# Kernel optimization log

Hardware: AMD Instinct MI355X
Metric: run time of the kernel (lower is better)

Reference implementation:

```python
import jax, jax.numpy as jnp
import numpy as np

B, L, F, C, H, FF = 8, 64, 16, 128, 8, 512


def setup_inputs() -> dict:
    key = jax.random.key(0)
    ks = jax.random.split(key, 5)
    s = jnp.float32(0.02)
    return {
        "x": jax.random.normal(ks[0], (B, L, F, C), jnp.float32),
        "wq": jax.random.normal(ks[1], (C * H, C), jnp.float32) * s,
        "bq": jnp.zeros((C * H,), jnp.float32),
        "wk": jax.random.normal(ks[2], (C * H, C), jnp.float32) * s,
        "bk": jnp.zeros((C * H,), jnp.float32),
        "wv": jax.random.normal(ks[3], (C * H, C), jnp.float32) * s,
        "bv": jnp.zeros((C * H,), jnp.float32),
        "wo": jax.random.normal(ks[4], (C, C * H), jnp.float32) * s,
        "bo": jnp.zeros((C,), jnp.float32),
        "ln1_g": jnp.ones((C,), jnp.float32),
        "ln1_b": jnp.zeros((C,), jnp.float32),
        "w1": jax.random.normal(jax.random.fold_in(key, 10), (FF, C), jnp.float32) * s,
        "b1": jnp.zeros((FF,), jnp.float32),
        "w2": jax.random.normal(jax.random.fold_in(key, 11), (C, FF), jnp.float32) * s,
        "b2": jnp.zeros((C,), jnp.float32),
        "ln2_g": jnp.ones((C,), jnp.float32),
        "ln2_b": jnp.zeros((C,), jnp.float32),
    }


def _layer_norm(x, g, b, eps=1e-5):
    m = jnp.mean(x, axis=-1, keepdims=True)
    v = jnp.mean(jnp.square(x - m), axis=-1, keepdims=True)  # biased var, like torch LN
    return (x - m) * jax.lax.rsqrt(v + eps) * g + b


def reference(x, wq, bq, wk, bk, wv, bv, wo, bo, ln1_g, ln1_b, w1, b1, w2, b2, ln2_g, ln2_b):
    b_, l, f, c = x.shape
    h = wq.shape[0] // c  # num_heads

    def proj(w, bias):
        y = x @ w.T + bias                       # (B,L,F,C*H)
        y = y.reshape(b_, l, f, c, h)
        return jnp.transpose(y, (0, 4, 1, 2, 3))  # (B,H,L,F,C)

    q = proj(wq, bq)
    k = proj(wk, bk)
    v = proj(wv, bv)

    # scores over joint (L,F) query/key axes: (B,H,Lq,Fq,Lk,Fk)
    scores = jnp.einsum('bhlfc,bhmgc->bhlfmg', q, k) / jnp.sqrt(jnp.float32(c))
    # double softmax: first over key-L axis, then over key-F axis of the result
    a = jax.nn.softmax(scores, axis=4)
    a = jax.nn.softmax(a, axis=5)
    z = jnp.einsum('bhlfmg,bhmgc->bhlfc', a, v)   # (B,H,L,F,C)
    z = jnp.transpose(z, (0, 2, 3, 4, 1)).reshape(b_, l, f, c * h)
    attn_out = z @ wo.T + bo                      # (B,L,F,C)

    z1 = _layer_norm(attn_out + x, ln1_g, ln1_b)  # residual + LN1 (dropout=0, eval)
    ffy = jax.nn.relu(z1 @ w1.T + b1) @ w2.T + b2
    return _layer_norm(ffy + z1, ln2_g, ln2_b)
```

## Files before the change

### kernel.cpp

```cpp
#include <hip/hip_runtime.h>


typedef unsigned short u16;
typedef unsigned int u32;
typedef __attribute__((ext_vector_type(4))) float f32x4;
typedef __attribute__((ext_vector_type(8))) short s16x8;
typedef __attribute__((ext_vector_type(4))) unsigned short u16x4;

__device__ __forceinline__ u16 f2bf(float f) {
    union { float f; u32 u; } v; v.f = f;
    u32 u = v.u;
    u += 0x7fffu + ((u >> 16) & 1u);
    return (u16)(u >> 16);
}
__device__ __forceinline__ float bf2f(u16 h) {
    union { u32 u; float f; } v; v.u = ((u32)h) << 16;
    return v.f;
}
__device__ __forceinline__ u32 pack_trunc(float lo, float hi) {
    return __builtin_amdgcn_perm(__float_as_uint(hi), __float_as_uint(lo), 0x07060302u);
}
__device__ __forceinline__ s16x8 ldg8(const u16* p) { return *(const s16x8*)p; }

#define MFMA(a, b, c) __builtin_amdgcn_mfma_f32_16x16x32_bf16((a), (b), (c), 0, 0, 0)

__global__ __launch_bounds__(256) void k_prep(
    const float* __restrict__ x, const float* __restrict__ wq,
    const float* __restrict__ wk, const float* __restrict__ wv,
    const float* __restrict__ wo, const float* __restrict__ w1,
    const float* __restrict__ w2,
    u16* __restrict__ Xb, u16* __restrict__ Wqb, u16* __restrict__ Wkb,
    u16* __restrict__ Wvb, u16* __restrict__ Wob, u16* __restrict__ W1b,
    u16* __restrict__ W2b)
{
    int i = blockIdx.x * 256 + threadIdx.x;
    if (i < 360448) {
        int v = i * 4;
        float4 f; u16* dst; size_t addr;
        if (v < 1048576) {
            int t = v >> 7, k = v & 127;
            f = *(const float4*)(x + v);
            dst = Xb;
            addr = (size_t)((t >> 4) * 4 + (k >> 5)) * 512 + (t & 15) * 32 + (k & 31);
        } else {
            int v2 = v - 1048576;
            int w = v2 >> 17, off = v2 & 131071;
            const float* src = (w == 0) ? wq : (w == 1) ? wk : wv;
            dst = (w == 0) ? Wqb : (w == 1) ? Wkb : Wvb;
            int o = off >> 7, k = off & 127;
            int h = o & 7, cp = o >> 3;
            f = *(const float4*)(src + off);
            addr = (size_t)((h * 8 + (cp >> 4)) * 4 + (k >> 5)) * 512 + (cp & 15) * 32 + (k & 31);
        }
        u16x4 o4; o4.x = f2bf(f.x); o4.y = f2bf(f.y); o4.z = f2bf(f.z); o4.w = f2bf(f.w);
        *(u16x4*)(dst + addr) = o4;
    } else {
        int i2 = i - 360448;
        if (i2 < 131072) {
            int n = i2 >> 10, o2 = i2 & 1023;
            int h = o2 >> 7, c = o2 & 127;
            size_t addr = (size_t)((n >> 4) * 32 + (o2 >> 5)) * 512 + (n & 15) * 32 + (o2 & 31);
            Wob[addr] = f2bf(wo[n * 1024 + c * 8 + h]);
        } else {
            int v = (i2 - 131072) * 4;
            float4 f; u16* dst; size_t addr;
            if (v < 65536) {
                int o = v >> 7, k = v & 127;
                f = *(const float4*)(w1 + v);
                dst = W1b;
                addr = (size_t)((o >> 4) * 4 + (k >> 5)) * 512 + (o & 15) * 32 + (k & 31);
            } else {
                int v2 = v - 65536;
                int n = v2 >> 9, k = v2 & 511;
                f = *(const float4*)(w2 + v2);
                dst = W2b;
                addr = (size_t)((n >> 4) * 16 + (k >> 5)) * 512 + (n & 15) * 32 + (k & 31);
            }
            u16x4 o4; o4.x = f2bf(f.x); o4.y = f2bf(f.y); o4.z = f2bf(f.z); o4.w = f2bf(f.w);
            *(u16x4*)(dst + addr) = o4;
        }
    }
}

__global__ __launch_bounds__(256) void k_qkv(
    const u16* __restrict__ Xb,
    const u16* __restrict__ Wqb, const u16* __restrict__ Wkb, const u16* __restrict__ Wvb,
    const float* __restrict__ bq, const float* __restrict__ bk, const float* __restrict__ bv,
    u16* __restrict__ Qblk, u16* __restrict__ Kblk, u16* __restrict__ Vblk)
{
    const int tid = threadIdx.x, lane = tid & 63, wid = tid >> 6;
    const int colb = lane & 15, quad = lane >> 4;
    const int fl = colb * 32 + quad * 8;
    const int t0 = blockIdx.x * 128;
    const int cb = blockIdx.y;
    const int h = cb >> 1, c0 = (cb & 1) * 64;

    const u16* at0 = Xb + (size_t)((t0 >> 4) + wid * 2) * 2048 + fl;
    const u16* at1 = at0 + 2048;
    s16x8 a0[4], a1[4];
    #pragma unroll
    for (int i = 0; i < 4; ++i) { a0[i] = ldg8(at0 + i * 512); a1[i] = ldg8(at1 + i * 512); }

    #pragma unroll
    for (int gz = 0; gz < 3; ++gz) {
        const u16* W = (gz == 0) ? Wqb : (gz == 1) ? Wkb : Wvb;
        const float* bias = (gz == 0) ? bq : (gz == 1) ? bk : bv;
        f32x4 acc[2][4] = {};
        #pragma unroll
        for (int j = 0; j < 4; ++j) {
            int cpt = (c0 >> 4) + j;
            const u16* bt = W + (size_t)((h * 8 + cpt) * 4) * 512 + fl;
            #pragma unroll
            for (int i = 0; i < 4; ++i) {
                s16x8 b = ldg8(bt + i * 512);
                acc[0][j] = MFMA(a0[i], b, acc[0][j]);
                acc[1][j] = MFMA(a1[i], b, acc[1][j]);
            }
        }
        #pragma unroll
        for (int rt = 0; rt < 2; ++rt) {
            #pragma unroll
            for (int j = 0; j < 4; ++j) {
                int cpr = c0 + j * 16 + colb;
                float bs = bias[cpr * 8 + h];
                if (gz < 2) {
                    u16* dst = (gz == 0) ? Qblk : Kblk;
                    #pragma unroll
                    for (int r = 0; r < 4; ++r) {
                        int t = t0 + (wid * 2 + rt) * 16 + quad * 4 + r;
                        int bi = t >> 10, rr = t & 1023;
                        size_t addr = (size_t)(bi * 8 + h) * 131072
                                    + (size_t)((rr >> 4) * 4 + (cpr >> 5)) * 512
                                    + (rr & 15) * 32 + (cpr & 31);
                        dst[addr] = f2bf(acc[rt][j][r] + bs);
                    }
                } else {
                    int t = t0 + (wid * 2 + rt) * 16 + quad * 4;
                    int bi = t >> 10, rr = t & 1023;
                    size_t addr = (size_t)(bi * 8 + h) * 131072
                                + (size_t)((cpr >> 4) * 32 + (rr >> 5)) * 512
                                + (cpr & 15) * 32 + (rr & 31);
                    u16x4 o;
                    o.x = f2bf(acc[rt][j][0] + bs); o.y = f2bf(acc[rt][j][1] + bs);
                    o.z = f2bf(acc[rt][j][2] + bs); o.w = f2bf(acc[rt][j][3] + bs);
                    *(u16x4*)&Vblk[addr] = o;
                }
            }
        }
    }
}

__global__ __launch_bounds__(512, 4) void k_attn(
    const u16* __restrict__ Qblk, const u16* __restrict__ Kblk, const u16* __restrict__ Vblk,
    u16* __restrict__ Zblk)
{
    __shared__ u16 sS[32 * 1032];
    __shared__ float sZsum[32][16];
    __shared__ float sZi[32][20];

    const int tid = threadIdx.x, lane = tid & 63, wid = tid >> 6;
    const int colb = lane & 15, quad = lane >> 4;
    const int fl = colb * 32 + quad * 8;
    const int bid = blockIdx.x;
    const int bh = (bid & 7) + 8 * ((bid >> 3) & 7);
    const int r0 = (bid >> 6) * 32;
    const size_t qkb = (size_t)bh * 131072;
    const float SCALE = 0.08838834764831845f;

    sZsum[tid >> 4][tid & 15] = 0.f;
    __syncthreads();

    const u16* qt = Qblk + qkb + (size_t)(r0 >> 4) * 2048 + fl;
    s16x8 aq[2][4];
    #pragma unroll
    for (int mt = 0; mt < 2; ++mt)
        #pragma unroll
        for (int i = 0; i < 4; ++i)
            aq[mt][i] = ldg8(qt + mt * 2048 + i * 512);

    const u16* kt0 = Kblk + qkb + (size_t)wid * 2048 + fl;
    float zs[2][4] = {};
    s16x8 kc[4], kn[4];
    #pragma unroll
    for (int i = 0; i < 4; ++i) kc[i] = ldg8(kt0 + i * 512);
    #pragma unroll
    for (int j = 0; j < 8; ++j) {
        if (j < 7) {
            const u16* kp = kt0 + (size_t)(8 * (j + 1)) * 2048;
            #pragma unroll
            for (int i = 0; i < 4; ++i) kn[i] = ldg8(kp + i * 512);
        }
        f32x4 ac0 = {}, ac1 = {};
        ac0 = MFMA(aq[0][0], kc[0], ac0); ac1 = MFMA(aq[1][0], kc[0], ac1);
        ac0 = MFMA(aq[0][1], kc[1], ac0); ac1 = MFMA(aq[1][1], kc[1], ac1);
        ac0 = MFMA(aq[0][2], kc[2], ac0); ac1 = MFMA(aq[1][2], kc[2], ac1);
        ac0 = MFMA(aq[0][3], kc[3], ac0); ac1 = MFMA(aq[1][3], kc[3], ac1);
        const int kt = wid + 8 * j;
        #pragma unroll
        for (int r = 0; r < 4; ++r) {
            int row0 = quad * 4 + r;
            float p0 = __expf(ac0[r] * SCALE);
            float p1 = __expf(ac1[r] * SCALE);
            u32 u0 = __float_as_uint(p0), u1 = __float_as_uint(p1);
            zs[0][r] += __uint_as_float(u0 & 0xffff0000u);
            zs[1][r] += __uint_as_float(u1 & 0xffff0000u);
            sS[row0 * 1032 + kt * 16 + colb] = (u16)(u0 >> 16);
            sS[(16 + row0) * 1032 + kt * 16 + colb] = (u16)(u1 >> 16);
        }
        #pragma unroll
        for (int i = 0; i < 4; ++i) kc[i] = kn[i];
    }
    #pragma unroll
    for (int mt = 0; mt < 2; ++mt)
        #pragma unroll
        for (int r = 0; r < 4; ++r)
            atomicAdd(&sZsum[mt * 16 + quad * 4 + r][colb], zs[mt][r]);
    __syncthreads();

    {
        int row = tid >> 4, g = tid & 15;
        sZi[row][g] = 1.0f / sZsum[row][g];
    }
    __syncthreads();

    {
        const int row = tid & 31, mb = (tid >> 5) * 4;
        float zi[16];
        #pragma unroll
        for (int i = 0; i < 4; ++i) {
            f32x4 z4 = *(const f32x4*)&sZi[row][i * 4];
            zi[i*4] = z4[0]; zi[i*4+1] = z4[1]; zi[i*4+2] = z4[2]; zi[i*4+3] = z4[3];
        }
        #pragma unroll
        for (int tk = 0; tk < 4; ++tk) {
            int m = mb + tk;
            u16* base = &sS[row * 1032 + m * 16];
            s16x8 pa = *(const s16x8*)base;
            s16x8 pb = *(const s16x8*)(base + 8);
            float w[16]; float sum = 0.f;
            #pragma unroll
            for (int g = 0; g < 8; ++g) {
                w[g] = __expf(bf2f((u16)pa[g]) * zi[g]);      sum += w[g];
                w[g+8] = __expf(bf2f((u16)pb[g]) * zi[g+8]);  sum += w[g+8];
            }
            float inv = 1.0f / sum;
            u32 o[8];
            #pragma unroll
            for (int g = 0; g < 8; ++g)
                o[g] = pack_trunc(w[2*g] * inv, w[2*g+1] * inv);
            *(u32*)(base + 0)  = o[0]; *(u32*)(base + 2)  = o[1];
            *(u32*)(base + 4)  = o[2]; *(u32*)(base + 6)  = o[3];
            *(u32*)(base + 8)  = o[4]; *(u32*)(base + 10) = o[5];
            *(u32*)(base + 12) = o[6]; *(u32*)(base + 14) = o[7];
        }
    }
    __syncthreads();

    f32x4 zac[2] = {};
    const u16* aS0 = &sS[colb * 1032 + quad * 8];
    const u16* aS1 = aS0 + 16 * 1032;
    const u16* vt = Vblk + qkb + (size_t)wid * 16384 + fl;
    #pragma unroll
    for (int c = 0; c < 8; ++c) {
        s16x8 v[4];
        #pragma unroll
        for (int i = 0; i < 4; ++i) v[i] = ldg8(vt + (c * 4 + i) * 512);
        #pragma unroll
        for (int i = 0; i < 4; ++i) {
            int kk = (c * 4 + i) * 32;
            zac[0] = MFMA(*(const s16x8*)(aS0 + kk), v[i], zac[0]);
            zac[1] = MFMA(*(const s16x8*)(aS1 + kk), v[i], zac[1]);
        }
    }
    const int bi = bh >> 3, hh = bh & 7;
    const int tt = (bi * 1024 + r0) >> 4;
    #pragma unroll
    for (int mt = 0; mt < 2; ++mt) {
        size_t base = (size_t)((tt + mt) * 32 + hh * 4 + (wid >> 1)) * 512
                    + (wid & 1) * 16 + colb;
        #pragma unroll
        for (int r = 0; r < 4; ++r)
            Zblk[base + (quad * 4 + r) * 32] = f2bf(zac[mt][r]);
    }
}

__global__ __launch_bounds__(512, 2) void k_tail(
    const u16* __restrict__ Zblk, const u16* __restrict__ Wob, const float* __restrict__ bo,
    const float* __restrict__ x,  const float* __restrict__ g1, const float* __restrict__ be1,
    const u16* __restrict__ W1b, const float* __restrict__ b1,
    const u16* __restrict__ W2b, const float* __restrict__ b2,
    const float* __restrict__ g2, const float* __restrict__ be2,
    float* __restrict__ out)
{
    __shared__ float sC[32][132];
    __shared__ float sZ1f[32][132];
    __shared__ u16  sZ1h[32][136];
    __shared__ u16  sH[32][520];
    const int tid = threadIdx.x, lane = tid & 63, w = tid >> 6;
    const int colb = lane & 15, quad = lane >> 4;
    const int fl = colb * 32 + quad * 8;
    const int t0 = blockIdx.x * 32;

    {
        const u16* at0 = Zblk + (size_t)(blockIdx.x * 2) * 16384 + fl;
        const u16* at1 = at0 + 16384;
        const u16* bt = Wob + (size_t)w * 16384 + fl;
        f32x4 acc0 = {}, acc1 = {};
        #pragma unroll
        for (int kt = 0; kt < 32; ++kt) {
            s16x8 b = ldg8(bt + kt * 512);
            acc0 = MFMA(ldg8(at0 + kt * 512), b, acc0);
            acc1 = MFMA(ldg8(at1 + kt * 512), b, acc1);
        }
        #pragma unroll
        for (int r = 0; r < 4; ++r) {
            sC[quad * 4 + r][w * 16 + colb] = acc0[r];
            sC[16 + quad * 4 + r][w * 16 + colb] = acc1[r];
        }
    }
    __syncthreads();

    {
        const int row = tid >> 4, cg = tid & 15;
        float v[8];
        {
            f32x4 s0 = *(const f32x4*)&sC[row][cg * 8];
            f32x4 s1 = *(const f32x4*)&sC[row][cg * 8 + 4];
            float4 x0 = *(const float4*)&x[(size_t)(t0 + row) * 128 + cg * 8];
            float4 x1 = *(const float4*)&x[(size_t)(t0 + row) * 128 + cg * 8 + 4];
            float4 b0 = *(const float4*)&bo[cg * 8];
            float4 b1v = *(const float4*)&bo[cg * 8 + 4];
            v[0] = s0[0]+b0.x+x0.x; v[1] = s0[1]+b0.y+x0.y;
            v[2] = s0[2]+b0.z+x0.z; v[3] = s0[3]+b0.w+x0.w;
            v[4] = s1[0]+b1v.x+x1.x; v[5] = s1[1]+b1v.y+x1.y;
            v[6] = s1[2]+b1v.z+x1.z; v[7] = s1[3]+b1v.w+x1.w;
        }
        float s = v[0]+v[1]+v[2]+v[3]+v[4]+v[5]+v[6]+v[7];
        s += __shfl_xor(s, 1); s += __shfl_xor(s, 2);
        s += __shfl_xor(s, 4); s += __shfl_xor(s, 8);
        float mean = s * (1.0f / 128.0f);
        float d, vs = 0.f;
        #pragma unroll
        for (int j = 0; j < 8; ++j) { d = v[j] - mean; vs += d * d; }
        vs += __shfl_xor(vs, 1); vs += __shfl_xor(vs, 2);
        vs += __shfl_xor(vs, 4); vs += __shfl_xor(vs, 8);
        float rstd = rsqrtf(vs * (1.0f / 128.0f) + 1e-5f);
        float4 gg0 = *(const float4*)&g1[cg * 8], gg1 = *(const float4*)&g1[cg * 8 + 4];
        float4 bb0 = *(const float4*)&be1[cg * 8], bb1 = *(const float4*)&be1[cg * 8 + 4];
        float z[8];
        z[0]=(v[0]-mean)*rstd*gg0.x+bb0.x; z[1]=(v[1]-mean)*rstd*gg0.y+bb0.y;
        z[2]=(v[2]-mean)*rstd*gg0.z+bb0.z; z[3]=(v[3]-mean)*rstd*gg0.w+bb0.w;
        z[4]=(v[4]-mean)*rstd*gg1.x+bb1.x; z[5]=(v[5]-mean)*rstd*gg1.y+bb1.y;
        z[6]=(v[6]-mean)*rstd*gg1.z+bb1.z; z[7]=(v[7]-mean)*rstd*gg1.w+bb1.w;
        *(f32x4*)&sZ1f[row][cg * 8]     = (f32x4){z[0], z[1], z[2], z[3]};
        *(f32x4*)&sZ1f[row][cg * 8 + 4] = (f32x4){z[4], z[5], z[6], z[7]};
        u16x4 h0, h1;
        h0.x=f2bf(z[0]); h0.y=f2bf(z[1]); h0.z=f2bf(z[2]); h0.w=f2bf(z[3]);
        h1.x=f2bf(z[4]); h1.y=f2bf(z[5]); h1.z=f2bf(z[6]); h1.w=f2bf(z[7]);
        *(u16x4*)&sZ1h[row][cg * 8] = h0;
        *(u16x4*)&sZ1h[row][cg * 8 + 4] = h1;
    }
    __syncthreads();

    {
        s16x8 bz0[4], bz1[4];
        #pragma unroll
        for (int i = 0; i < 4; ++i) {
            bz0[i] = *(const s16x8*)&sZ1h[colb][quad * 8 + i * 32];
            bz1[i] = *(const s16x8*)&sZ1h[16 + colb][quad * 8 + i * 32];
        }
        #pragma unroll
        for (int ot = 0; ot < 4; ++ot) {
            const u16* wt = W1b + (size_t)((w * 4 + ot) * 4) * 512 + fl;
            s16x8 wf0 = ldg8(wt), wf1 = ldg8(wt + 512);
            s16x8 wf2 = ldg8(wt + 1024), wf3 = ldg8(wt + 1536);
            f32x4 a0 = {}, a1 = {};
            a0 = MFMA(wf0, bz0[0], a0); a1 = MFMA(wf0, bz1[0], a1);
            a0 = MFMA(wf1, bz0[1], a0); a1 = MFMA(wf1, bz1[1], a1);
            a0 = MFMA(wf2, bz0[2], a0); a1 = MFMA(wf2, bz1[2], a1);
            a0 = MFMA(wf3, bz0[3], a0); a1 = MFMA(wf3, bz1[3], a1);
            int o = (w * 4 + ot) * 16 + quad * 4;
            float4 bs = *(const float4*)&b1[o];
            u16x4 hv0, hv1;
            hv0.x = f2bf(fmaxf(a0[0] + bs.x, 0.f));
            hv0.y = f2bf(fmaxf(a0[1] + bs.y, 0.f));
            hv0.z = f2bf(fmaxf(a0[2] + bs.z, 0.f));
            hv0.w = f2bf(fmaxf(a0[3] + bs.w, 0.f));
            hv1.x = f2bf(fmaxf(a1[0] + bs.x, 0.f));
            hv1.y = f2bf(fmaxf(a1[1] + bs.y, 0.f));
            hv1.z = f2bf(fmaxf(a1[2] + bs.z, 0.f));
            hv1.w = f2bf(fmaxf(a1[3] + bs.w, 0.f));
            *(u16x4*)&sH[colb][o] = hv0;
            *(u16x4*)&sH[16 + colb][o] = hv1;
        }
    }
    __syncthreads();

    {
        const u16* bt = W2b + (size_t)w * 8192 + fl;
        f32x4 acc0 = {}, acc1 = {};
        #pragma unroll
        for (int kt = 0; kt < 16; ++kt) {
            s16x8 b = ldg8(bt + kt * 512);
            s16x8 a0 = *(const s16x8*)&sH[colb][quad * 8 + kt * 32];
            s16x8 a1 = *(const s16x8*)&sH[16 + colb][quad * 8 + kt * 32];
            acc0 = MFMA(a0, b, acc0);
            acc1 = MFMA(a1, b, acc1);
        }
        #pragma unroll
        for (int r = 0; r < 4; ++r) {
            sC[quad * 4 + r][w * 16 + colb] = acc0[r];
            sC[16 + quad * 4 + r][w * 16 + colb] = acc1[r];
        }
    }
    __syncthreads();

    {
        const int row = tid >> 4, cg = tid & 15;
        float v[8];
        {
            f32x4 s0 = *(const f32x4*)&sC[row][cg * 8];
            f32x4 s1 = *(const f32x4*)&sC[row][cg * 8 + 4];
            f32x4 z0 = *(const f32x4*)&sZ1f[row][cg * 8];
            f32x4 z1 = *(const f32x4*)&sZ1f[row][cg * 8 + 4];
            float4 b0 = *(const float4*)&b2[cg * 8];
            float4 b1v = *(const float4*)&b2[cg * 8 + 4];
            v[0] = s0[0]+b0.x+z0[0]; v[1] = s0[1]+b0.y+z0[1];
            v[2] = s0[2]+b0.z+z0[2]; v[3] = s0[3]+b0.w+z0[3];
            v[4] = s1[0]+b1v.x+z1[0]; v[5] = s1[1]+b1v.y+z1[1];
            v[6] = s1[2]+b1v.z+z1[2]; v[7] = s1[3]+b1v.w+z1[3];
        }
        float s = v[0]+v[1]+v[2]+v[3]+v[4]+v[5]+v[6]+v[7];
        s += __shfl_xor(s, 1); s += __shfl_xor(s, 2);
        s += __shfl_xor(s, 4); s += __shfl_xor(s, 8);
        float mean = s * (1.0f / 128.0f);
        float d, vs = 0.f;
        #pragma unroll
        for (int j = 0; j < 8; ++j) { d = v[j] - mean; vs += d * d; }
        vs += __shfl_xor(vs, 1); vs += __shfl_xor(vs, 2);
        vs += __shfl_xor(vs, 4); vs += __shfl_xor(vs, 8);
        float rstd = rsqrtf(vs * (1.0f / 128.0f) + 1e-5f);
        float4 gg0 = *(const float4*)&g2[cg * 8], gg1 = *(const float4*)&g2[cg * 8 + 4];
        float4 bb0 = *(const float4*)&be2[cg * 8], bb1 = *(const float4*)&be2[cg * 8 + 4];
        size_t ob = (size_t)(t0 + row) * 128 + cg * 8;
        *(float4*)&out[ob] = make_float4(
            (v[0]-mean)*rstd*gg0.x+bb0.x, (v[1]-mean)*rstd*gg0.y+bb0.y,
            (v[2]-mean)*rstd*gg0.z+bb0.z, (v[3]-mean)*rstd*gg0.w+bb0.w);
        *(float4*)&out[ob + 4] = make_float4(
            (v[4]-mean)*rstd*gg1.x+bb1.x, (v[5]-mean)*rstd*gg1.y+bb1.y,
            (v[6]-mean)*rstd*gg1.z+bb1.z, (v[7]-mean)*rstd*gg1.w+bb1.w);
    }
}

extern "C" void kernel_launch(void* const* d_in, const int* in_sizes, int n_in,
                              void* d_out, int out_size, void* d_ws, size_t ws_size,
                              hipStream_t stream)
{
    (void)in_sizes; (void)n_in; (void)out_size; (void)ws_size;
    const float* x   = (const float*)d_in[0];
    const float* wq  = (const float*)d_in[1];
    const float* bq  = (const float*)d_in[2];
    const float* wk  = (const float*)d_in[3];
    const float* bk  = (const float*)d_in[4];
    const float* wv  = (const float*)d_in[5];
    const float* bv  = (const float*)d_in[6];
    const float* wo  = (const float*)d_in[7];
    const float* bo  = (const float*)d_in[8];
    const float* g1  = (const float*)d_in[9];
    const float* be1 = (const float*)d_in[10];
    const float* w1  = (const float*)d_in[11];
    const float* b1  = (const float*)d_in[12];
    const float* w2  = (const float*)d_in[13];
    const float* b2  = (const float*)d_in[14];
    const float* g2  = (const float*)d_in[15];
    const float* be2 = (const float*)d_in[16];

    char* ws = (char*)d_ws;
    const size_t MB = (size_t)1 << 20;
    u16*   Qblk = (u16*)(ws + 0 * MB);
    u16*   Kblk = (u16*)(ws + 16 * MB);
    u16*   Vblk = (u16*)(ws + 32 * MB);
    u16*   Zblk = (u16*)(ws + 48 * MB);
    u16*   Xb  = (u16*)(ws + 48 * MB);
    u16*   Wqb = (u16*)(ws + 50 * MB);
    u16*   Wkb = (u16*)(ws + 50 * MB + 262144);
    u16*   Wvb = (u16*)(ws + 50 * MB + 524288);
    u16*   Wob = (u16*)(ws + 64 * MB);
    u16*   W1b = (u16*)(ws + 64 * MB + 524288);
    u16*   W2b = (u16*)(ws + 64 * MB + 786432);
    float* out = (float*)d_out;

    k_prep<<<2048, 256, 0, stream>>>(x, wq, wk, wv, wo, w1, w2,
                                     Xb, Wqb, Wkb, Wvb, Wob, W1b, W2b);
    k_qkv<<<dim3(64, 16), 256, 0, stream>>>(Xb, Wqb, Wkb, Wvb, bq, bk, bv, Qblk, Kblk, Vblk);
    k_attn<<<2048, 512, 0, stream>>>(Qblk, Kblk, Vblk, Zblk);
    k_tail<<<256, 512, 0, stream>>>(Zblk, Wob, bo, x, g1, be1, W1b, b1, W2b, b2, g2, be2, out);
}
```

Before: 240.1 us.

## Switch attention Q/K/V and probability tiles to FP8 MFMA with offset encoding

```diff
diff --git a/kernel.cpp b/kernel.cpp
--- a/kernel.cpp
+++ b/kernel.cpp
@@ -2,7 +2,10 @@
 
 
 typedef unsigned short u16;
+typedef unsigned char u8;
 typedef unsigned int u32;
+typedef long long i64;
+typedef __attribute__((ext_vector_type(2))) float f32x2;
 typedef __attribute__((ext_vector_type(4))) float f32x4;
 typedef __attribute__((ext_vector_type(8))) short s16x8;
 typedef __attribute__((ext_vector_type(4))) unsigned short u16x4;
@@ -13,16 +16,14 @@
     u += 0x7fffu + ((u >> 16) & 1u);
     return (u16)(u >> 16);
 }
-__device__ __forceinline__ float bf2f(u16 h) {
-    union { u32 u; float f; } v; v.u = ((u32)h) << 16;
-    return v.f;
-}
-__device__ __forceinline__ u32 pack_trunc(float lo, float hi) {
-    return __builtin_amdgcn_perm(__float_as_uint(hi), __float_as_uint(lo), 0x07060302u);
-}
 __device__ __forceinline__ s16x8 ldg8(const u16* p) { return *(const s16x8*)p; }
-
-#define MFMA(a, b, c) __builtin_amdgcn_mfma_f32_16x16x32_bf16((a), (b), (c), 0, 0, 0)
+__device__ __forceinline__ i64 ld64(const u8* p) { return *(const i64*)p; }
+__device__ __forceinline__ u8 f2fp8(float v) {
+    return (u8)((u32)__builtin_amdgcn_cvt_pk_fp8_f32(v, v, 0, false) & 0xffu);
+}
+
+#define MFMA(a, b, c)  __builtin_amdgcn_mfma_f32_16x16x32_bf16((a), (b), (c), 0, 0, 0)
+#define MFMA8(a, b, c) __builtin_amdgcn_mfma_f32_16x16x32_fp8_fp8((a), (b), (c), 0, 0, 0)
 
 __global__ __launch_bounds__(256) void k_prep(
     const float* __restrict__ x, const float* __restrict__ wq,
@@ -31,7 +32,7 @@
     const float* __restrict__ w2,
     u16* __restrict__ Xb, u16* __restrict__ Wqb, u16* __restrict__ Wkb,
     u16* __restrict__ Wvb, u16* __restrict__ Wob, u16* __restrict__ W1b,
-    u16* __restrict__ W2b)
+    u16* __restrict__ W2b, float* __restrict__ Vcol)
 {
     int i = blockIdx.x * 256 + threadIdx.x;
     if (i < 360448) {
@@ -54,7 +55,7 @@
         }
         u16x4 o4; o4.x = f2bf(f.x); o4.y = f2bf(f.y); o4.z = f2bf(f.z); o4.w = f2bf(f.w);
         *(u16x4*)(dst + addr) = o4;
-    } else {
+    } else if (i < 524288) {
         int i2 = i - 360448;
         if (i2 < 131072) {
             int n = i2 >> 10, o2 = i2 & 1023;
@@ -79,6 +80,9 @@
             u16x4 o4; o4.x = f2bf(f.x); o4.y = f2bf(f.y); o4.z = f2bf(f.z); o4.w = f2bf(f.w);
             *(u16x4*)(dst + addr) = o4;
         }
+    } else {
+        int vz = i - 524288;
+        if (vz < 8192) Vcol[vz] = 0.f;
     }
 }
 
@@ -86,7 +90,8 @@
     const u16* __restrict__ Xb,
     const u16* __restrict__ Wqb, const u16* __restrict__ Wkb, const u16* __restrict__ Wvb,
     const float* __restrict__ bq, const float* __restrict__ bk, const float* __restrict__ bv,
-    u16* __restrict__ Qblk, u16* __restrict__ Kblk, u16* __restrict__ Vblk)
+    u8* __restrict__ Qblk, u8* __restrict__ Kblk, u8* __restrict__ Vblk,
+    float* __restrict__ Vcol)
 {
     const int tid = threadIdx.x, lane = tid & 63, wid = tid >> 6;
     const int colb = lane & 15, quad = lane >> 4;
@@ -94,6 +99,7 @@
     const int t0 = blockIdx.x * 128;
     const int cb = blockIdx.y;
     const int h = cb >> 1, c0 = (cb & 1) * 64;
+    const int bi = t0 >> 10;
 
     const u16* at0 = Xb + (size_t)((t0 >> 4) + wid * 2) * 2048 + fl;
     const u16* at1 = at0 + 2048;
@@ -124,39 +130,46 @@
                 int cpr = c0 + j * 16 + colb;
                 float bs = bias[cpr * 8 + h];
                 if (gz < 2) {
-                    u16* dst = (gz == 0) ? Qblk : Kblk;
+                    u8* dst = (gz == 0) ? Qblk : Kblk;
                     #pragma unroll
                     for (int r = 0; r < 4; ++r) {
                         int t = t0 + (wid * 2 + rt) * 16 + quad * 4 + r;
-                        int bi = t >> 10, rr = t & 1023;
+                        int rr = t & 1023;
                         size_t addr = (size_t)(bi * 8 + h) * 131072
                                     + (size_t)((rr >> 4) * 4 + (cpr >> 5)) * 512
                                     + (rr & 15) * 32 + (cpr & 31);
-                        dst[addr] = f2bf(acc[rt][j][r] + bs);
+                        dst[addr] = f2fp8(acc[rt][j][r] + bs);
                     }
                 } else {
                     int t = t0 + (wid * 2 + rt) * 16 + quad * 4;
-                    int bi = t >> 10, rr = t & 1023;
+                    int rr = t & 1023;
                     size_t addr = (size_t)(bi * 8 + h) * 131072
                                 + (size_t)((cpr >> 4) * 32 + (rr >> 5)) * 512
                                 + (cpr & 15) * 32 + (rr & 31);
-                    u16x4 o;
-                    o.x = f2bf(acc[rt][j][0] + bs); o.y = f2bf(acc[rt][j][1] + bs);
-                    o.z = f2bf(acc[rt][j][2] + bs); o.w = f2bf(acc[rt][j][3] + bs);
-                    *(u16x4*)&Vblk[addr] = o;
+                    float v0 = acc[rt][j][0] + bs, v1 = acc[rt][j][1] + bs;
+                    float v2 = acc[rt][j][2] + bs, v3 = acc[rt][j][3] + bs;
+                    u32 o = 0;
+                    o = (u32)__builtin_amdgcn_cvt_pk_fp8_f32(v0, v1, o, false);
+                    o = (u32)__builtin_amdgcn_cvt_pk_fp8_f32(v2, v3, o, true);
+                    *(u32*)&Vblk[addr] = o;
+                    float s = v0 + v1 + v2 + v3;
+                    s += __shfl_xor(s, 16);
+                    s += __shfl_xor(s, 32);
+                    if (quad == 0)
+                        atomicAdd(&Vcol[(bi * 8 + h) * 128 + cpr], s);
                 }
             }
         }
     }
 }
 
-__global__ __launch_bounds__(512, 4) void k_attn(
-    const u16* __restrict__ Qblk, const u16* __restrict__ Kblk, const u16* __restrict__ Vblk,
-    u16* __restrict__ Zblk)
+__global__ __launch_bounds__(512, 8) void k_attn(
+    const u8* __restrict__ Qblk, const u8* __restrict__ Kblk, const u8* __restrict__ Vblk,
+    const float* __restrict__ Vcol, u16* __restrict__ Zblk)
 {
-    __shared__ u16 sS[32 * 1032];
+    __shared__ u8 sS8[32 * 1040];
     __shared__ float sZsum[32][16];
-    __shared__ float sZi[32][20];
+    __shared__ float sZi[32][17];
 
     const int tid = threadIdx.x, lane = tid & 63, wid = tid >> 6;
     const int colb = lane & 15, quad = lane >> 4;
@@ -170,45 +183,37 @@
     sZsum[tid >> 4][tid & 15] = 0.f;
     __syncthreads();
 
-    const u16* qt = Qblk + qkb + (size_t)(r0 >> 4) * 2048 + fl;
-    s16x8 aq[2][4];
+    const u8* qt = Qblk + qkb + (size_t)(r0 >> 4) * 2048 + fl;
+    i64 aq[2][4];
     #pragma unroll
     for (int mt = 0; mt < 2; ++mt)
         #pragma unroll
         for (int i = 0; i < 4; ++i)
-            aq[mt][i] = ldg8(qt + mt * 2048 + i * 512);
-
-    const u16* kt0 = Kblk + qkb + (size_t)wid * 2048 + fl;
+            aq[mt][i] = ld64(qt + mt * 2048 + i * 512);
+
+    const u8* kt0 = Kblk + qkb + (size_t)wid * 2048 + fl;
     float zs[2][4] = {};
-    s16x8 kc[4], kn[4];
-    #pragma unroll
-    for (int i = 0; i < 4; ++i) kc[i] = ldg8(kt0 + i * 512);
     #pragma unroll
     for (int j = 0; j < 8; ++j) {
-        if (j < 7) {
-            const u16* kp = kt0 + (size_t)(8 * (j + 1)) * 2048;
-            #pragma unroll
-            for (int i = 0; i < 4; ++i) kn[i] = ldg8(kp + i * 512);
-        }
+        const u8* kp = kt0 + (size_t)(8 * j) * 2048;
+        i64 k0 = ld64(kp), k1 = ld64(kp + 512), k2 = ld64(kp + 1024), k3 = ld64(kp + 1536);
         f32x4 ac0 = {}, ac1 = {};
-        ac0 = MFMA(aq[0][0], kc[0], ac0); ac1 = MFMA(aq[1][0], kc[0], ac1);
-        ac0 = MFMA(aq[0][1], kc[1], ac0); ac1 = MFMA(aq[1][1], kc[1], ac1);
-        ac0 = MFMA(aq[0][2], kc[2], ac0); ac1 = MFMA(aq[1][2], kc[2], ac1);
-        ac0 = MFMA(aq[0][3], kc[3], ac0); ac1 = MFMA(aq[1][3], kc[3], ac1);
+        ac0 = MFMA8(aq[0][0], k0, ac0); ac1 = MFMA8(aq[1][0], k0, ac1);
+        ac0 = MFMA8(aq[0][1], k1, ac0); ac1 = MFMA8(aq[1][1], k1, ac1);
+        ac0 = MFMA8(aq[0][2], k2, ac0); ac1 = MFMA8(aq[1][2], k2, ac1);
+        ac0 = MFMA8(aq[0][3], k3, ac0); ac1 = MFMA8(aq[1][3], k3, ac1);
         const int kt = wid + 8 * j;
         #pragma unroll
         for (int r = 0; r < 4; ++r) {
             int row0 = quad * 4 + r;
             float p0 = __expf(ac0[r] * SCALE);
             float p1 = __expf(ac1[r] * SCALE);
-            u32 u0 = __float_as_uint(p0), u1 = __float_as_uint(p1);
-            zs[0][r] += __uint_as_float(u0 & 0xffff0000u);
-            zs[1][r] += __uint_as_float(u1 & 0xffff0000u);
-            sS[row0 * 1032 + kt * 16 + colb] = (u16)(u0 >> 16);
-            sS[(16 + row0) * 1032 + kt * 16 + colb] = (u16)(u1 >> 16);
-        }
-        #pragma unroll
-        for (int i = 0; i < 4; ++i) kc[i] = kn[i];
+            zs[0][r] += p0; zs[1][r] += p1;
+            u32 pk = (u32)__builtin_amdgcn_cvt_pk_fp8_f32(
+                         (p0 - 1.0f) * 8.0f, (p1 - 1.0f) * 8.0f, 0, false);
+            sS8[row0 * 1040 + kt * 16 + colb] = (u8)(pk & 0xffu);
+            sS8[(16 + row0) * 1040 + kt * 16 + colb] = (u8)((pk >> 8) & 0xffu);
+        }
     }
     #pragma unroll
     for (int mt = 0; mt < 2; ++mt)
@@ -217,70 +222,73 @@
             atomicAdd(&sZsum[mt * 16 + quad * 4 + r][colb], zs[mt][r]);
     __syncthreads();
 
-    {
-        int row = tid >> 4, g = tid & 15;
-        sZi[row][g] = 1.0f / sZsum[row][g];
-    }
+    sZi[tid >> 4][tid & 15] = 1.0f / sZsum[tid >> 4][tid & 15];
     __syncthreads();
 
     {
         const int row = tid & 31, mb = (tid >> 5) * 4;
         float zi[16];
         #pragma unroll
-        for (int i = 0; i < 4; ++i) {
-            f32x4 z4 = *(const f32x4*)&sZi[row][i * 4];
-            zi[i*4] = z4[0]; zi[i*4+1] = z4[1]; zi[i*4+2] = z4[2]; zi[i*4+3] = z4[3];
-        }
+        for (int g = 0; g < 16; ++g) zi[g] = sZi[row][g];
         #pragma unroll
         for (int tk = 0; tk < 4; ++tk) {
             int m = mb + tk;
-            u16* base = &sS[row * 1032 + m * 16];
-            s16x8 pa = *(const s16x8*)base;
-            s16x8 pb = *(const s16x8*)(base + 8);
+            u32* bp = (u32*)&sS8[row * 1040 + m * 16];
             float w[16]; float sum = 0.f;
             #pragma unroll
-            for (int g = 0; g < 8; ++g) {
-                w[g] = __expf(bf2f((u16)pa[g]) * zi[g]);      sum += w[g];
-                w[g+8] = __expf(bf2f((u16)pb[g]) * zi[g+8]);  sum += w[g+8];
+            for (int q4 = 0; q4 < 4; ++q4) {
+                u32 ww = bp[q4];
+                f32x2 eA = __builtin_amdgcn_cvt_pk_f32_fp8(ww, false);
+                f32x2 eB = __builtin_amdgcn_cvt_pk_f32_fp8(ww, true);
+                int g = q4 * 4;
+                w[g+0] = __expf(zi[g+0] * fmaf(eA[0], 0.125f, 1.0f)); sum += w[g+0];
+                w[g+1] = __expf(zi[g+1] * fmaf(eA[1], 0.125f, 1.0f)); sum += w[g+1];
+                w[g+2] = __expf(zi[g+2] * fmaf(eB[0], 0.125f, 1.0f)); sum += w[g+2];
+                w[g+3] = __expf(zi[g+3] * fmaf(eB[1], 0.125f, 1.0f)); sum += w[g+3];
             }
-            float inv = 1.0f / sum;
-            u32 o[8];
+            float inv1024 = 1024.0f / sum;
             #pragma unroll
-            for (int g = 0; g < 8; ++g)
-                o[g] = pack_trunc(w[2*g] * inv, w[2*g+1] * inv);
-            *(u32*)(base + 0)  = o[0]; *(u32*)(base + 2)  = o[1];
-            *(u32*)(base + 4)  = o[2]; *(u32*)(base + 6)  = o[3];
-            *(u32*)(base + 8)  = o[4]; *(u32*)(base + 10) = o[5];
-            *(u32*)(base + 12) = o[6]; *(u32*)(base + 14) = o[7];
+            for (int q4 = 0; q4 < 4; ++q4) {
+                int g = q4 * 4;
+                u32 o = 0;
+                o = (u32)__builtin_amdgcn_cvt_pk_fp8_f32(
+                        fmaf(w[g+0], inv1024, -64.f), fmaf(w[g+1], inv1024, -64.f), o, false);
+                o = (u32)__builtin_amdgcn_cvt_pk_fp8_f32(
+                        fmaf(w[g+2], inv1024, -64.f), fmaf(w[g+3], inv1024, -64.f), o, true);
+                bp[q4] = o;
+            }
         }
     }
     __syncthreads();
 
     f32x4 zac[2] = {};
-    const u16* aS0 = &sS[colb * 1032 + quad * 8];
-    const u16* aS1 = aS0 + 16 * 1032;
-    const u16* vt = Vblk + qkb + (size_t)wid * 16384 + fl;
+    const u8* aS0 = &sS8[colb * 1040 + quad * 8];
+    const u8* aS1 = aS0 + 16 * 1040;
+    const u8* vt = Vblk + qkb + (size_t)wid * 16384 + fl;
     #pragma unroll
     for (int c = 0; c < 8; ++c) {
-        s16x8 v[4];
-        #pragma unroll
-        for (int i = 0; i < 4; ++i) v[i] = ldg8(vt + (c * 4 + i) * 512);
         #pragma unroll
         for (int i = 0; i < 4; ++i) {
-            int kk = (c * 4 + i) * 32;
-            zac[0] = MFMA(*(const s16x8*)(aS0 + kk), v[i], zac[0]);
-            zac[1] = MFMA(*(const s16x8*)(aS1 + kk), v[i], zac[1]);
+            int mtile = c * 4 + i;
+            i64 v = ld64(vt + mtile * 512);
+            i64 s0 = *(const i64*)(aS0 + mtile * 32);
+            i64 s1 = *(const i64*)(aS1 + mtile * 32);
+            zac[0] = MFMA8(s0, v, zac[0]);
+            zac[1] = MFMA8(s1, v, zac[1]);
         }
     }
     const int bi = bh >> 3, hh = bh & 7;
     const int tt = (bi * 1024 + r0) >> 4;
+    const float vsum = Vcol[bh * 128 + wid * 16 + colb];
     #pragma unroll
     for (int mt = 0; mt < 2; ++mt) {
         size_t base = (size_t)((tt + mt) * 32 + hh * 4 + (wid >> 1)) * 512
                     + (wid & 1) * 16 + colb;
         #pragma unroll
-        for (int r = 0; r < 4; ++r)
-            Zblk[base + (quad * 4 + r) * 32] = f2bf(zac[mt][r]);
+        for (int r = 0; r < 4; ++r) {
+            float z = fmaf(zac[mt][r], 0.0009765625f, vsum * 0.0625f);
+            Zblk[base + (quad * 4 + r) * 32] = f2bf(z);
+        }
     }
 }
 
@@ -477,22 +485,24 @@
 
     char* ws = (char*)d_ws;
     const size_t MB = (size_t)1 << 20;
-    u16*   Qblk = (u16*)(ws + 0 * MB);
-    u16*   Kblk = (u16*)(ws + 16 * MB);
-    u16*   Vblk = (u16*)(ws + 32 * MB);
+    u8*    Qblk = (u8*)(ws + 0 * MB);
+    u8*    Kblk = (u8*)(ws + 16 * MB);
+    u8*    Vblk = (u8*)(ws + 32 * MB);
     u16*   Zblk = (u16*)(ws + 48 * MB);
     u16*   Xb  = (u16*)(ws + 48 * MB);
     u16*   Wqb = (u16*)(ws + 50 * MB);
     u16*   Wkb = (u16*)(ws + 50 * MB + 262144);
     u16*   Wvb = (u16*)(ws + 50 * MB + 524288);
-    u16*   Wob = (u16*)(ws + 64 * MB);
-    u16*   W1b = (u16*)(ws + 64 * MB + 524288);
-    u16*   W2b = (u16*)(ws + 64 * MB + 786432);
+    u16*   Wob  = (u16*)(ws + 64 * MB);
+    u16*   W1b  = (u16*)(ws + 64 * MB + 524288);
+    u16*   W2b  = (u16*)(ws + 64 * MB + 786432);
+    float* Vcol = (float*)(ws + 65 * MB);
     float* out = (float*)d_out;
 
-    k_prep<<<2048, 256, 0, stream>>>(x, wq, wk, wv, wo, w1, w2,
-                                     Xb, Wqb, Wkb, Wvb, Wob, W1b, W2b);
-    k_qkv<<<dim3(64, 16), 256, 0, stream>>>(Xb, Wqb, Wkb, Wvb, bq, bk, bv, Qblk, Kblk, Vblk);
-    k_attn<<<2048, 512, 0, stream>>>(Qblk, Kblk, Vblk, Zblk);
+    k_prep<<<2080, 256, 0, stream>>>(x, wq, wk, wv, wo, w1, w2,
+                                     Xb, Wqb, Wkb, Wvb, Wob, W1b, W2b, Vcol);
+    k_qkv<<<dim3(64, 16), 256, 0, stream>>>(Xb, Wqb, Wkb, Wvb, bq, bk, bv,
+                                            Qblk, Kblk, Vblk, Vcol);
+    k_attn<<<2048, 512, 0, stream>>>(Qblk, Kblk, Vblk, Vcol, Zblk);
     k_tail<<<256, 512, 0, stream>>>(Zblk, Wob, bo, x, g1, be1, W1b, b1, W2b, b2, g2, be2, out);
 }
```

Result: faster. 225.2 us (-6.2%).
